# Kernel optimization log

Measured on AMD Instinct MI355X. Metric: run time of the kernel, lower is better.

Reference implementation:

```python
import jax, jax.numpy as jnp
import numpy as np

K, D, B, T = 512, 256, 32, 4096

def setup_inputs() -> dict:
    key = jax.random.key(0)
    k1, k2 = jax.random.split(key)
    z_e_x = jax.random.normal(k1, (B, D, T), dtype=jnp.float32)
    # nn.Embedding weight init uniform(-1/K, 1/K)
    emb_weight = jax.random.uniform(k2, (K, D), dtype=jnp.float32, minval=-1.0 / K, maxval=1.0 / K)
    return {"z_e_x": z_e_x, "emb_weight": emb_weight}

def reference(z_e_x, emb_weight):
    # forward(): permute [B,D,T] -> [B,T,D], nearest-codebook indices
    z = jnp.transpose(z_e_x, (0, 2, 1))  # [B, T, D]
    # squared L2 distances: ||z||^2 - 2 z.W^T + ||W||^2  -> [B, T, K]
    z_sq = jnp.sum(z * z, axis=-1, keepdims=True)           # [B, T, 1]
    w_sq = jnp.sum(emb_weight * emb_weight, axis=-1)        # [K]
    cross = jnp.einsum('btd,kd->btk', z, emb_weight)        # [B, T, K]
    dists = z_sq - 2.0 * cross + w_sq[None, None, :]
    latents = jnp.argmin(dists, axis=-1)                    # [B, T] int
    return latents
```

## Files before the change

kernel.cpp:

```cpp
#include <hip/hip_runtime.h>
#include <math.h>

#define NK 512
#define DD 256
#define NB 32
#define NT 4096

typedef __attribute__((ext_vector_type(8))) short bf16x8;
typedef __attribute__((ext_vector_type(4))) float f32x4;

#define MARGIN 1.5e-4f
#define PAD 104

__device__ __forceinline__ void bsplit(float x, unsigned short& h, unsigned short& l) {
    unsigned int u = __float_as_uint(x);
    unsigned int r = u + 0x7fffu + ((u >> 16) & 1u);
    h = (unsigned short)(r >> 16);
    float hf = __uint_as_float(((unsigned int)h) << 16);
    float res = x - hf;
    unsigned int u2 = __float_as_uint(res);
    unsigned int r2 = u2 + 0x7fffu + ((u2 >> 16) & 1u);
    l = (unsigned short)(r2 >> 16);
}

__global__ __launch_bounds__(256) void wsq_kernel(const float* __restrict__ W,
                                                  float* __restrict__ wsq) {
    int k = blockIdx.x * blockDim.x + threadIdx.x;
    if (k >= NK) return;
    const float4* row = (const float4*)(W + (size_t)k * DD);
    double s = 0.0;
    #pragma unroll 8
    for (int i = 0; i < DD / 4; ++i) {
        float4 v = row[i];
        s += (double)v.x * v.x + (double)v.y * v.y + (double)v.z * v.z + (double)v.w * v.w;
    }
    wsq[k] = (float)s;
}

__global__ __launch_bounds__(512) void convw_kernel(const float* __restrict__ W,
                                                    unsigned short* __restrict__ Wpp) {
    const int c = blockIdx.x;
    const int k = threadIdx.x;
    const int d0 = c * 32;

    float w[32];
    const float4* src4 = (const float4*)(W + (size_t)k * DD + d0);
    #pragma unroll
    for (int q = 0; q < 8; ++q) {
        float4 v = src4[q];
        w[4 * q + 0] = v.x; w[4 * q + 1] = v.y; w[4 * q + 2] = v.z; w[4 * q + 3] = v.w;
    }
    __align__(16) unsigned short o[96];
    #pragma unroll
    for (int j = 0; j < 32; ++j) {
        unsigned short h, l;
        bsplit(w[j], h, l);
        o[3 * j + 0] = h;
        o[3 * j + 1] = l;
        o[3 * j + 2] = h;
    }
    unsigned short* dst = Wpp + ((size_t)c * 512 + k) * 96;
    #pragma unroll
    for (int j = 0; j < 12; ++j) ((int4*)dst)[j] = ((const int4*)o)[j];
}

__global__ void zero_cnt(int* cnt) {
    if (threadIdx.x == 0 && blockIdx.x == 0) *cnt = 0;
}

__global__ __launch_bounds__(256, 2) void vq_phase1(const float* __restrict__ Z,
                                                    const unsigned short* __restrict__ Wpp,
                                                    const float* __restrict__ wsq,
                                                    float* __restrict__ gq1,
                                                    float* __restrict__ gq2,
                                                    int* __restrict__ gi1) {
    __shared__ __align__(16) short As[128 * PAD];
    __shared__ __align__(16) short Bs[256 * PAD];

    const int tid  = threadIdx.x;
    const int wave = tid >> 6;
    const int lane = tid & 63;
    const int lm   = lane & 15;
    const int lq   = lane >> 4;
    const int mw   = wave & 1;
    const int nw   = wave >> 1;

    const int bx = blockIdx.x;
    const int h  = bx & 1;
    const int tl = bx >> 1;
    const int b  = tl >> 5;
    const int t0 = (tl & 31) * 128;

    const int t_l = tid & 127;
    const int dg  = tid >> 7;

    const float* zcol = Z + (size_t)b * DD * NT + t0 + t_l;

    f32x4 acc[4][8];
    #pragma unroll
    for (int mt = 0; mt < 4; ++mt)
        #pragma unroll
        for (int nt = 0; nt < 8; ++nt)
            acc[mt][nt] = (f32x4){0.f, 0.f, 0.f, 0.f};

    double zacc = 0.0;

    for (int c = 0; c < 8; ++c) {
        const int d0 = c * 32;
        __syncthreads();

        {
            float zv[16];
            #pragma unroll
            for (int j = 0; j < 16; ++j)
                zv[j] = zcol[(size_t)(d0 + dg * 16 + j) * NT];
            #pragma unroll
            for (int j = 0; j < 16; ++j)
                zacc = fma((double)zv[j], (double)zv[j], zacc);

            __align__(16) unsigned int u[24];
            #pragma unroll
            for (int p = 0; p < 8; ++p) {
                int j = 2 * p;
                unsigned short h0, l0, h1, l1;
                bsplit(zv[j], h0, l0);
                bsplit(zv[j + 1], h1, l1);
                u[3 * p + 0] = (unsigned int)h0 | ((unsigned int)h0 << 16);
                u[3 * p + 1] = (unsigned int)l0 | ((unsigned int)h1 << 16);
                u[3 * p + 2] = (unsigned int)h1 | ((unsigned int)l1 << 16);
            }
            int4* dst = (int4*)&As[t_l * PAD + dg * 48];
            #pragma unroll
            for (int q = 0; q < 6; ++q) dst[q] = ((const int4*)u)[q];
        }
        {
            const unsigned short* src = Wpp + ((size_t)c * 512 + h * 256 + tid) * 96;
            int4 v[12];
            #pragma unroll
            for (int j = 0; j < 12; ++j) v[j] = ((const int4*)src)[j];
            int4* bd = (int4*)&Bs[tid * PAD];
            #pragma unroll
            for (int j = 0; j < 12; ++j) bd[j] = v[j];
        }
        __syncthreads();

        #pragma unroll
        for (int ks = 0; ks < 3; ++ks) {
            bf16x8 a[4], bb[8];
            #pragma unroll
            for (int mt = 0; mt < 4; ++mt)
                a[mt] = *(const bf16x8*)&As[(mw * 64 + mt * 16 + lm) * PAD + ks * 32 + lq * 8];
            #pragma unroll
            for (int nt = 0; nt < 8; ++nt)
                bb[nt] = *(const bf16x8*)&Bs[(nw * 128 + nt * 16 + lm) * PAD + ks * 32 + lq * 8];
            #pragma unroll
            for (int mt = 0; mt < 4; ++mt)
                #pragma unroll
                for (int nt = 0; nt < 8; ++nt)
                    acc[mt][nt] = __builtin_amdgcn_mfma_f32_16x16x32_bf16(
                        a[mt], bb[nt], acc[mt][nt], 0, 0, 0);
        }
    }

    __syncthreads();
    double* zred = (double*)As;
    zred[dg * 128 + t_l] = zacc;
    __syncthreads();
    float* zf = (float*)Bs;
    if (tid < 128) zf[tid] = (float)(zred[tid] + zred[128 + tid]);
    __syncthreads();

    float wq[8];
    #pragma unroll
    for (int nt = 0; nt < 8; ++nt)
        wq[nt] = wsq[h * 256 + nw * 128 + nt * 16 + lm];
    const int kbase = h * 256 + nw * 128 + lm;

    float* cb1 = (float*)As;
    float* cb2 = cb1 + 256;
    int*   cbi = (int*)(cb2 + 256);

    #pragma unroll
    for (int mt = 0; mt < 4; ++mt) {
        #pragma unroll
        for (int r = 0; r < 4; ++r) {
            float zz = zf[mw * 64 + mt * 16 + lq * 4 + r];
            float q1 = INFINITY, q2 = INFINITY;
            int i1 = 0x7fffffff;
            #pragma unroll
            for (int nt = 0; nt < 8; ++nt) {
                float dist = __fadd_rn(__fsub_rn(zz, __fmul_rn(2.0f, acc[mt][nt][r])), wq[nt]);
                int kk = kbase + nt * 16;
                if (dist < q1 || (dist == q1 && kk < i1)) { q2 = q1; q1 = dist; i1 = kk; }
                else if (dist < q2) q2 = dist;
            }
            #pragma unroll
            for (int mk = 1; mk <= 8; mk <<= 1) {
                float o1 = __shfl_xor(q1, mk);
                float o2 = __shfl_xor(q2, mk);
                int   oi = __shfl_xor(i1, mk);
                if (o1 < q1 || (o1 == q1 && oi < i1)) { q2 = fminf(q1, o2); q1 = o1; i1 = oi; }
                else { q2 = fminf(o1, q2); }
            }
            if (lm == 0) {
                int m = mw * 64 + mt * 16 + lq * 4 + r;
                cb1[m * 2 + nw] = q1;
                cb2[m * 2 + nw] = q2;
                cbi[m * 2 + nw] = i1;
            }
        }
    }
    __syncthreads();
    if (tid < 128) {
        float a1 = cb1[tid * 2],     a2 = cb2[tid * 2];     int ai = cbi[tid * 2];
        float b1 = cb1[tid * 2 + 1], b2 = cb2[tid * 2 + 1]; int bi = cbi[tid * 2 + 1];
        float q1, q2; int i1;
        if (b1 < a1 || (b1 == a1 && bi < ai)) { q1 = b1; i1 = bi; q2 = fminf(a1, b2); }
        else { q1 = a1; i1 = ai; q2 = fminf(b1, a2); }
        size_t bt = (size_t)b * NT + t0 + tid;
        gq1[bt * 2 + h] = q1;
        gq2[bt * 2 + h] = q2;
        gi1[bt * 2 + h] = i1;
    }
}

__global__ __launch_bounds__(256) void vq_merge(const float* __restrict__ gq1,
                                                const float* __restrict__ gq2,
                                                const int* __restrict__ gi1,
                                                int* __restrict__ out,
                                                int* __restrict__ list,
                                                int* __restrict__ cnt) {
    const int bt = blockIdx.x * 256 + threadIdx.x;
    float a1 = gq1[(size_t)bt * 2],     a2 = gq2[(size_t)bt * 2];     int ai = gi1[(size_t)bt * 2];
    float b1 = gq1[(size_t)bt * 2 + 1], b2 = gq2[(size_t)bt * 2 + 1]; int bi = gi1[(size_t)bt * 2 + 1];
    float q1, q2; int i1;
    if (b1 < a1 || (b1 == a1 && bi < ai)) { q1 = b1; i1 = bi; q2 = fminf(a1, b2); }
    else { q1 = a1; i1 = ai; q2 = fminf(b1, a2); }
    out[bt] = i1;
    if (q2 - q1 <= MARGIN) {
        int idx = atomicAdd(cnt, 1);
        list[idx] = bt;
    }
}

__global__ __launch_bounds__(256) void vq_fix(const float* __restrict__ Z,
                                              const float* __restrict__ W,
                                              const float* __restrict__ wsq,
                                              const int* __restrict__ list,
                                              const int* __restrict__ cnt,
                                              int* __restrict__ out) {
    __shared__ float  Zs[8][256];
    __shared__ double pz[8][32];
    __shared__ float  zsqs[8];
    __shared__ int    bts[8];
    __shared__ float  rv[8][4];
    __shared__ int    ri[8][4];

    const int n    = *cnt;
    const int tid  = threadIdx.x;
    const int lane = tid & 63;
    const int wv   = tid >> 6;

    for (int base = blockIdx.x * 8; base < n; base += gridDim.x * 8) {
        const int m = (n - base < 8) ? (n - base) : 8;
        __syncthreads();
        if (tid < 8) bts[tid] = list[base + ((tid < m) ? tid : 0)];
        __syncthreads();

        #pragma unroll
        for (int i = 0; i < 8; ++i) {
            if (i < m) {
                int bt = bts[i];
                int bb = bt >> 12, t = bt & 4095;
                Zs[i][tid] = Z[(size_t)bb * DD * NT + (size_t)tid * NT + t];
            }
        }
        __syncthreads();

        {
            int i = tid >> 5, seg = tid & 31;
            double s = 0.0;
            #pragma unroll
            for (int j = 0; j < 8; ++j) {
                double zz = (double)Zs[i][seg * 8 + j];
                s = fma(zz, zz, s);
            }
            pz[i][seg] = s;
        }
        __syncthreads();
        if (tid < 8) {
            double s = 0.0;
            #pragma unroll
            for (int j = 0; j < 32; ++j) s += pz[tid][j];
            zsqs[tid] = (float)s;
        }
        __syncthreads();

        float da[2][8];
        #pragma unroll
        for (int rr = 0; rr < 2; ++rr) {
            int k = tid + rr * 256;
            const float4* wr = (const float4*)(W + (size_t)k * DD);
            float a8[8];
            #pragma unroll
            for (int i = 0; i < 8; ++i) a8[i] = 0.f;
            for (int q = 0; q < 64; ++q) {
                float4 w4 = wr[q];
                #pragma unroll
                for (int i = 0; i < 8; ++i) {
                    a8[i] = fmaf(Zs[i][4 * q + 0], w4.x, a8[i]);
                    a8[i] = fmaf(Zs[i][4 * q + 1], w4.y, a8[i]);
                    a8[i] = fmaf(Zs[i][4 * q + 2], w4.z, a8[i]);
                    a8[i] = fmaf(Zs[i][4 * q + 3], w4.w, a8[i]);
                }
            }
            float wqv = wsq[k];
            #pragma unroll
            for (int i = 0; i < 8; ++i)
                da[rr][i] = __fadd_rn(__fsub_rn(zsqs[i], __fmul_rn(2.0f, a8[i])), wqv);
        }

        #pragma unroll
        for (int i = 0; i < 8; ++i) {
            float v = da[0][i]; int ix = tid;
            if (da[1][i] < v) { v = da[1][i]; ix = tid + 256; }
            #pragma unroll
            for (int mk = 1; mk <= 32; mk <<= 1) {
                float ov = __shfl_xor(v, mk);
                int   oi = __shfl_xor(ix, mk);
                if (ov < v || (ov == v && oi < ix)) { v = ov; ix = oi; }
            }
            if (lane == 0) { rv[i][wv] = v; ri[i][wv] = ix; }
        }
        __syncthreads();
        if (tid < 8 && tid < m) {
            float v = INFINITY; int ix = 0x7fffffff;
            #pragma unroll
            for (int w = 0; w < 4; ++w) {
                if (rv[tid][w] < v || (rv[tid][w] == v && ri[tid][w] < ix)) {
                    v = rv[tid][w]; ix = ri[tid][w];
                }
            }
            out[bts[tid]] = ix;
        }
    }
}

#define BT 128
#define BK 128
#define DCHUNK 32
#define NKC (NK / BK)
#define NDC (DD / DCHUNK)
#define WSTR (BK + 4)

__global__ __launch_bounds__(256) void vq_fallback(const float* __restrict__ Z,
                                                   const float* __restrict__ W,
                                                   const float* __restrict__ wsq_g,
                                                   int* __restrict__ out) {
    __shared__ __align__(16) float Zs[DCHUNK * BT];
    __shared__ __align__(16) float Ws[DCHUNK * WSTR];
    __shared__ float wsqs[NK];

    const int tid = threadIdx.x;
    const int tx  = tid & 15;
    const int ty  = tid >> 4;
    const int b   = blockIdx.y;
    const int t0  = blockIdx.x * BT;

    if (wsq_g) {
        wsqs[tid]       = wsq_g[tid];
        wsqs[tid + 256] = wsq_g[tid + 256];
    } else {
        for (int k = tid; k < NK; k += 256) {
            const float4* row = (const float4*)(W + (size_t)k * DD);
            double s = 0.0;
            for (int i = 0; i < DD / 4; ++i) {
                float4 v = row[i];
                s += (double)v.x * v.x + (double)v.y * v.y + (double)v.z * v.z + (double)v.w * v.w;
            }
            wsqs[k] = (float)s;
        }
    }

    const float* Zb = Z + (size_t)b * DD * NT + t0;

    float best[8]; int bidx[8];
    #pragma unroll
    for (int a = 0; a < 8; ++a) { best[a] = INFINITY; bidx[a] = 0x7fffffff; }
    double zsqd[8];
    #pragma unroll
    for (int a = 0; a < 8; ++a) zsqd[a] = 0.0;
    float zsqf[8];

    for (int kc = 0; kc < NKC; ++kc) {
        float acc[8][8];
        #pragma unroll
        for (int a = 0; a < 8; ++a)
            #pragma unroll
            for (int c = 0; c < 8; ++c) acc[a][c] = 0.f;

        for (int dc = 0; dc < NDC; ++dc) {
            const int d0 = dc * DCHUNK;
            __syncthreads();
            #pragma unroll
            for (int i = 0; i < 4; ++i) {
                int f  = tid + i * 256;
                int r  = f >> 5;
                int c4 = f & 31;
                float4 v = *(const float4*)(Zb + (size_t)(d0 + r) * NT + c4 * 4);
                *(float4*)(&Zs[r * BT + c4 * 4]) = v;
            }
            #pragma unroll
            for (int i = 0; i < 4; ++i) {
                int u  = tid + i * 256;
                int k  = u >> 3;
                int rg = u & 7;
                float4 v = *(const float4*)(W + (size_t)(kc * BK + k) * DD + d0 + rg * 4);
                Ws[(rg * 4 + 0) * WSTR + k] = v.x;
                Ws[(rg * 4 + 1) * WSTR + k] = v.y;
                Ws[(rg * 4 + 2) * WSTR + k] = v.z;
                Ws[(rg * 4 + 3) * WSTR + k] = v.w;
            }
            __syncthreads();
            #pragma unroll 4
            for (int d = 0; d < DCHUNK; ++d) {
                float4 z0 = *(const float4*)(&Zs[d * BT + ty * 8]);
                float4 z1 = *(const float4*)(&Zs[d * BT + ty * 8 + 4]);
                float4 w0 = *(const float4*)(&Ws[d * WSTR + tx * 8]);
                float4 w1 = *(const float4*)(&Ws[d * WSTR + tx * 8 + 4]);
                float za[8] = {z0.x, z0.y, z0.z, z0.w, z1.x, z1.y, z1.z, z1.w};
                float wa[8] = {w0.x, w0.y, w0.z, w0.w, w1.x, w1.y, w1.z, w1.w};
                if (kc == 0) {
                    #pragma unroll
                    for (int a = 0; a < 8; ++a)
                        zsqd[a] = fma((double)za[a], (double)za[a], zsqd[a]);
                }
                #pragma unroll
                for (int a = 0; a < 8; ++a)
                    #pragma unroll
                    for (int c = 0; c < 8; ++c)
                        acc[a][c] = fmaf(za[a], wa[c], acc[a][c]);
            }
        }
        if (kc == 0) {
            #pragma unroll
            for (int a = 0; a < 8; ++a) zsqf[a] = (float)zsqd[a];
        }
        #pragma unroll
        for (int c = 0; c < 8; ++c) {
            int   kg = kc * BK + tx * 8 + c;
            float wqv = wsqs[kg];
            #pragma unroll
            for (int a = 0; a < 8; ++a) {
                float c2   = __fmul_rn(2.0f, acc[a][c]);
                float s    = __fsub_rn(zsqf[a], c2);
                float dist = __fadd_rn(s, wqv);
                if (dist < best[a] || (dist == best[a] && kg < bidx[a])) {
                    best[a] = dist; bidx[a] = kg;
                }
            }
        }
    }
    __syncthreads();
    float* redv = Zs;
    int*   redi = (int*)Ws;
    #pragma unroll
    for (int a = 0; a < 8; ++a) {
        int tl2 = ty * 8 + a;
        redv[tl2 * 16 + tx] = best[a];
        redi[tl2 * 16 + tx] = bidx[a];
    }
    __syncthreads();
    if (tid < BT) {
        float bv = INFINITY; int bi = 0x7fffffff;
        #pragma unroll
        for (int j = 0; j < 16; ++j) {
            float v = redv[tid * 16 + j];
            int   i = redi[tid * 16 + j];
            if (v < bv || (v == bv && i < bi)) { bv = v; bi = i; }
        }
        out[(size_t)b * NT + t0 + tid] = bi;
    }
}

extern "C" void kernel_launch(void* const* d_in, const int* in_sizes, int n_in,
                              void* d_out, int out_size, void* d_ws, size_t ws_size,
                              hipStream_t stream) {
    const float* Z = (const float*)d_in[0];
    const float* W = (const float*)d_in[1];
    int* out = (int*)d_out;

    const size_t OFF_WSQ  = 0;
    const size_t OFF_CNT  = 2048;
    const size_t OFF_LIST = 4096;
    const size_t OFF_WPP  = OFF_LIST + 524288;
    const size_t OFF_GQ1  = OFF_WPP + 786432;
    const size_t OFF_GQ2  = OFF_GQ1 + 1048576;
    const size_t OFF_GI1  = OFF_GQ2 + 1048576;
    const size_t NEED     = OFF_GI1 + 1048576;

    if (ws_size >= NEED) {
        float* wsq = (float*)((char*)d_ws + OFF_WSQ);
        int*   cnt = (int*)((char*)d_ws + OFF_CNT);
        int*   list = (int*)((char*)d_ws + OFF_LIST);
        unsigned short* wpp = (unsigned short*)((char*)d_ws + OFF_WPP);
        float* gq1 = (float*)((char*)d_ws + OFF_GQ1);
        float* gq2 = (float*)((char*)d_ws + OFF_GQ2);
        int*   gi1 = (int*)((char*)d_ws + OFF_GI1);

        wsq_kernel<<<dim3(2), dim3(256), 0, stream>>>(W, wsq);
        convw_kernel<<<dim3(8), dim3(512), 0, stream>>>(W, wpp);
        zero_cnt<<<dim3(1), dim3(64), 0, stream>>>(cnt);
        vq_phase1<<<dim3(2048), dim3(256), 0, stream>>>(Z, wpp, wsq, gq1, gq2, gi1);
        vq_merge<<<dim3(512), dim3(256), 0, stream>>>(gq1, gq2, gi1, out, list, cnt);
        vq_fix<<<dim3(1024), dim3(256), 0, stream>>>(Z, W, wsq, list, cnt, out);
    } else {
        float* wsq = nullptr;
        if (ws_size >= NK * sizeof(float)) {
            wsq = (float*)d_ws;
            wsq_kernel<<<dim3(2), dim3(256), 0, stream>>>(W, wsq);
        }
        vq_fallback<<<dim3(NT / BT, NB), dim3(256), 0, stream>>>(Z, W, wsq, out);
    }
}
```

Before: 406.7 us.

## Switch to scaled fp16 two-term split and fuse merge with fix kernel

```diff
diff --git a/kernel.cpp b/kernel.cpp
--- a/kernel.cpp
+++ b/kernel.cpp
@@ -6,66 +6,55 @@
 #define NB 32
 #define NT 4096
 
-typedef __attribute__((ext_vector_type(8))) short bf16x8;
+typedef __attribute__((ext_vector_type(8))) _Float16 f16x8;
 typedef __attribute__((ext_vector_type(4))) float f32x4;
 
 #define MARGIN 1.5e-4f
-#define PAD 104
-
-__device__ __forceinline__ void bsplit(float x, unsigned short& h, unsigned short& l) {
-    unsigned int u = __float_as_uint(x);
-    unsigned int r = u + 0x7fffu + ((u >> 16) & 1u);
-    h = (unsigned short)(r >> 16);
-    float hf = __uint_as_float(((unsigned int)h) << 16);
-    float res = x - hf;
-    unsigned int u2 = __float_as_uint(res);
-    unsigned int r2 = u2 + 0x7fffu + ((u2 >> 16) & 1u);
-    l = (unsigned short)(r2 >> 16);
-}
-
-__global__ __launch_bounds__(256) void wsq_kernel(const float* __restrict__ W,
-                                                  float* __restrict__ wsq) {
-    int k = blockIdx.x * blockDim.x + threadIdx.x;
-    if (k >= NK) return;
-    const float4* row = (const float4*)(W + (size_t)k * DD);
-    double s = 0.0;
-    #pragma unroll 8
-    for (int i = 0; i < DD / 4; ++i) {
-        float4 v = row[i];
-        s += (double)v.x * v.x + (double)v.y * v.y + (double)v.z * v.z + (double)v.w * v.w;
-    }
-    wsq[k] = (float)s;
-}
-
-__global__ __launch_bounds__(512) void convw_kernel(const float* __restrict__ W,
-                                                    unsigned short* __restrict__ Wpp) {
-    const int c = blockIdx.x;
-    const int k = threadIdx.x;
-    const int d0 = c * 32;
-
-    float w[32];
-    const float4* src4 = (const float4*)(W + (size_t)k * DD + d0);
-    #pragma unroll
-    for (int q = 0; q < 8; ++q) {
-        float4 v = src4[q];
-        w[4 * q + 0] = v.x; w[4 * q + 1] = v.y; w[4 * q + 2] = v.z; w[4 * q + 3] = v.w;
-    }
-    __align__(16) unsigned short o[96];
-    #pragma unroll
-    for (int j = 0; j < 32; ++j) {
-        unsigned short h, l;
-        bsplit(w[j], h, l);
-        o[3 * j + 0] = h;
-        o[3 * j + 1] = l;
-        o[3 * j + 2] = h;
-    }
-    unsigned short* dst = Wpp + ((size_t)c * 512 + k) * 96;
-    #pragma unroll
-    for (int j = 0; j < 12; ++j) ((int4*)dst)[j] = ((const int4*)o)[j];
-}
-
-__global__ void zero_cnt(int* cnt) {
-    if (threadIdx.x == 0 && blockIdx.x == 0) *cnt = 0;
+#define DCH 16
+#define NCH 16
+#define KPC 32
+#define APAD 40
+
+__device__ __forceinline__ unsigned short f16bits(float x) {
+    _Float16 h = (_Float16)x;
+    unsigned short s;
+    __builtin_memcpy(&s, &h, 2);
+    return s;
+}
+
+__global__ __launch_bounds__(512) void prep_kernel(const float* __restrict__ W,
+                                                   unsigned short* __restrict__ Wpp,
+                                                   float* __restrict__ wsq) {
+    const int bx = blockIdx.x;
+    const int k  = threadIdx.x;
+    if (bx < NCH) {
+        const int d0 = bx * DCH;
+        float w[16];
+        const float4* src4 = (const float4*)(W + (size_t)k * DD + d0);
+        #pragma unroll
+        for (int q = 0; q < 4; ++q) {
+            float4 v = src4[q];
+            w[4 * q + 0] = v.x; w[4 * q + 1] = v.y; w[4 * q + 2] = v.z; w[4 * q + 3] = v.w;
+        }
+        __align__(16) unsigned int dw[16];
+        #pragma unroll
+        for (int j = 0; j < 16; ++j) {
+            unsigned short s = f16bits(w[j] * 4096.0f);
+            dw[j] = (unsigned int)s | ((unsigned int)s << 16);
+        }
+        unsigned short* dst = Wpp + ((size_t)bx * 512 + k) * 32;
+        #pragma unroll
+        for (int j = 0; j < 4; ++j) ((int4*)dst)[j] = ((const int4*)dw)[j];
+    } else {
+        const float4* row = (const float4*)(W + (size_t)k * DD);
+        double s = 0.0;
+        #pragma unroll 8
+        for (int i = 0; i < DD / 4; ++i) {
+            float4 v = row[i];
+            s += (double)v.x * v.x + (double)v.y * v.y + (double)v.z * v.z + (double)v.w * v.w;
+        }
+        wsq[k] = (float)s;
+    }
 }
 
 __global__ __launch_bounds__(256, 2) void vq_phase1(const float* __restrict__ Z,
@@ -74,8 +63,8 @@
                                                     float* __restrict__ gq1,
                                                     float* __restrict__ gq2,
                                                     int* __restrict__ gi1) {
-    __shared__ __align__(16) short As[128 * PAD];
-    __shared__ __align__(16) short Bs[256 * PAD];
+    __shared__ __align__(16) short As[128 * APAD];
+    __shared__ __align__(16) short Bs[256 * APAD];
 
     const int tid  = threadIdx.x;
     const int wave = tid >> 6;
@@ -105,61 +94,57 @@
 
     double zacc = 0.0;
 
-    for (int c = 0; c < 8; ++c) {
-        const int d0 = c * 32;
+    for (int c = 0; c < NCH; ++c) {
+        const int d0 = c * DCH;
         __syncthreads();
 
         {
-            float zv[16];
-            #pragma unroll
-            for (int j = 0; j < 16; ++j)
-                zv[j] = zcol[(size_t)(d0 + dg * 16 + j) * NT];
-            #pragma unroll
-            for (int j = 0; j < 16; ++j)
+            float zv[8];
+            #pragma unroll
+            for (int j = 0; j < 8; ++j)
+                zv[j] = zcol[(size_t)(d0 + dg * 8 + j) * NT];
+            #pragma unroll
+            for (int j = 0; j < 8; ++j)
                 zacc = fma((double)zv[j], (double)zv[j], zacc);
 
-            __align__(16) unsigned int u[24];
-            #pragma unroll
-            for (int p = 0; p < 8; ++p) {
-                int j = 2 * p;
-                unsigned short h0, l0, h1, l1;
-                bsplit(zv[j], h0, l0);
-                bsplit(zv[j + 1], h1, l1);
-                u[3 * p + 0] = (unsigned int)h0 | ((unsigned int)h0 << 16);
-                u[3 * p + 1] = (unsigned int)l0 | ((unsigned int)h1 << 16);
-                u[3 * p + 2] = (unsigned int)h1 | ((unsigned int)l1 << 16);
-            }
-            int4* dst = (int4*)&As[t_l * PAD + dg * 48];
-            #pragma unroll
-            for (int q = 0; q < 6; ++q) dst[q] = ((const int4*)u)[q];
+            __align__(16) unsigned int u[8];
+            #pragma unroll
+            for (int j = 0; j < 8; ++j) {
+                _Float16 zh = (_Float16)zv[j];
+                float rz = zv[j] - (float)zh;
+                unsigned short hs, ls;
+                __builtin_memcpy(&hs, &zh, 2);
+                ls = f16bits(rz);
+                u[j] = (unsigned int)hs | ((unsigned int)ls << 16);
+            }
+            int4* dst = (int4*)&As[t_l * APAD + dg * 16];
+            dst[0] = ((const int4*)u)[0];
+            dst[1] = ((const int4*)u)[1];
         }
         {
-            const unsigned short* src = Wpp + ((size_t)c * 512 + h * 256 + tid) * 96;
-            int4 v[12];
-            #pragma unroll
-            for (int j = 0; j < 12; ++j) v[j] = ((const int4*)src)[j];
-            int4* bd = (int4*)&Bs[tid * PAD];
-            #pragma unroll
-            for (int j = 0; j < 12; ++j) bd[j] = v[j];
-        }
-        __syncthreads();
-
-        #pragma unroll
-        for (int ks = 0; ks < 3; ++ks) {
-            bf16x8 a[4], bb[8];
-            #pragma unroll
-            for (int mt = 0; mt < 4; ++mt)
-                a[mt] = *(const bf16x8*)&As[(mw * 64 + mt * 16 + lm) * PAD + ks * 32 + lq * 8];
+            const unsigned short* src = Wpp + ((size_t)c * 512 + h * 256 + tid) * 32;
+            int4 v0 = ((const int4*)src)[0];
+            int4 v1 = ((const int4*)src)[1];
+            int4 v2 = ((const int4*)src)[2];
+            int4 v3 = ((const int4*)src)[3];
+            int4* bd = (int4*)&Bs[tid * APAD];
+            bd[0] = v0; bd[1] = v1; bd[2] = v2; bd[3] = v3;
+        }
+        __syncthreads();
+
+        f16x8 a[4], bb[8];
+        #pragma unroll
+        for (int mt = 0; mt < 4; ++mt)
+            a[mt] = *(const f16x8*)&As[(mw * 64 + mt * 16 + lm) * APAD + lq * 8];
+        #pragma unroll
+        for (int nt = 0; nt < 8; ++nt)
+            bb[nt] = *(const f16x8*)&Bs[(nw * 128 + nt * 16 + lm) * APAD + lq * 8];
+        #pragma unroll
+        for (int mt = 0; mt < 4; ++mt)
             #pragma unroll
             for (int nt = 0; nt < 8; ++nt)
-                bb[nt] = *(const bf16x8*)&Bs[(nw * 128 + nt * 16 + lm) * PAD + ks * 32 + lq * 8];
-            #pragma unroll
-            for (int mt = 0; mt < 4; ++mt)
-                #pragma unroll
-                for (int nt = 0; nt < 8; ++nt)
-                    acc[mt][nt] = __builtin_amdgcn_mfma_f32_16x16x32_bf16(
-                        a[mt], bb[nt], acc[mt][nt], 0, 0, 0);
-        }
+                acc[mt][nt] = __builtin_amdgcn_mfma_f32_16x16x32_f16(
+                    a[mt], bb[nt], acc[mt][nt], 0, 0, 0);
     }
 
     __syncthreads();
@@ -189,7 +174,8 @@
             int i1 = 0x7fffffff;
             #pragma unroll
             for (int nt = 0; nt < 8; ++nt) {
-                float dist = __fadd_rn(__fsub_rn(zz, __fmul_rn(2.0f, acc[mt][nt][r])), wq[nt]);
+                float c2   = __fmul_rn(acc[mt][nt][r], 4.8828125e-4f);
+                float dist = __fadd_rn(__fsub_rn(zz, c2), wq[nt]);
                 int kk = kbase + nt * 16;
                 if (dist < q1 || (dist == q1 && kk < i1)) { q2 = q1; q1 = dist; i1 = kk; }
                 else if (dist < q2) q2 = dist;
@@ -224,54 +210,56 @@
     }
 }
 
-__global__ __launch_bounds__(256) void vq_merge(const float* __restrict__ gq1,
-                                                const float* __restrict__ gq2,
-                                                const int* __restrict__ gi1,
-                                                int* __restrict__ out,
-                                                int* __restrict__ list,
-                                                int* __restrict__ cnt) {
-    const int bt = blockIdx.x * 256 + threadIdx.x;
-    float a1 = gq1[(size_t)bt * 2],     a2 = gq2[(size_t)bt * 2];     int ai = gi1[(size_t)bt * 2];
-    float b1 = gq1[(size_t)bt * 2 + 1], b2 = gq2[(size_t)bt * 2 + 1]; int bi = gi1[(size_t)bt * 2 + 1];
-    float q1, q2; int i1;
-    if (b1 < a1 || (b1 == a1 && bi < ai)) { q1 = b1; i1 = bi; q2 = fminf(a1, b2); }
-    else { q1 = a1; i1 = ai; q2 = fminf(b1, a2); }
-    out[bt] = i1;
-    if (q2 - q1 <= MARGIN) {
-        int idx = atomicAdd(cnt, 1);
-        list[idx] = bt;
-    }
-}
-
-__global__ __launch_bounds__(256) void vq_fix(const float* __restrict__ Z,
-                                              const float* __restrict__ W,
-                                              const float* __restrict__ wsq,
-                                              const int* __restrict__ list,
-                                              const int* __restrict__ cnt,
-                                              int* __restrict__ out) {
-    __shared__ float  Zs[8][256];
+__global__ __launch_bounds__(256) void vq_fixmerge(const float* __restrict__ Z,
+                                                   const float* __restrict__ W,
+                                                   const float* __restrict__ wsq,
+                                                   const float* __restrict__ gq1,
+                                                   const float* __restrict__ gq2,
+                                                   const int* __restrict__ gi1,
+                                                   int* __restrict__ out) {
+    __shared__ __align__(16) float Zs[8][256];
     __shared__ double pz[8][32];
     __shared__ float  zsqs[8];
     __shared__ int    bts[8];
     __shared__ float  rv[8][4];
     __shared__ int    ri[8][4];
-
-    const int n    = *cnt;
+    __shared__ int    lcnt;
+    __shared__ int    llist[256];
+
     const int tid  = threadIdx.x;
     const int lane = tid & 63;
     const int wv   = tid >> 6;
-
-    for (int base = blockIdx.x * 8; base < n; base += gridDim.x * 8) {
+    const int bt   = blockIdx.x * 256 + tid;
+
+    if (tid == 0) lcnt = 0;
+    __syncthreads();
+
+    {
+        float a1 = gq1[(size_t)bt * 2],     a2 = gq2[(size_t)bt * 2];     int ai = gi1[(size_t)bt * 2];
+        float b1 = gq1[(size_t)bt * 2 + 1], b2 = gq2[(size_t)bt * 2 + 1]; int bi = gi1[(size_t)bt * 2 + 1];
+        float q1, q2; int i1;
+        if (b1 < a1 || (b1 == a1 && bi < ai)) { q1 = b1; i1 = bi; q2 = fminf(a1, b2); }
+        else { q1 = a1; i1 = ai; q2 = fminf(b1, a2); }
+        out[bt] = i1;
+        if (q2 - q1 <= MARGIN) {
+            int p = atomicAdd(&lcnt, 1);
+            llist[p] = bt;
+        }
+    }
+    __syncthreads();
+    const int n = lcnt;
+
+    for (int base = 0; base < n; base += 8) {
         const int m = (n - base < 8) ? (n - base) : 8;
         __syncthreads();
-        if (tid < 8) bts[tid] = list[base + ((tid < m) ? tid : 0)];
+        if (tid < 8) bts[tid] = llist[base + ((tid < m) ? tid : 0)];
         __syncthreads();
 
         #pragma unroll
         for (int i = 0; i < 8; ++i) {
             if (i < m) {
-                int bt = bts[i];
-                int bb = bt >> 12, t = bt & 4095;
+                int tb = bts[i];
+                int bb = tb >> 12, t = tb & 4095;
                 Zs[i][tid] = Z[(size_t)bb * DD * NT + (size_t)tid * NT + t];
             }
         }
@@ -308,10 +296,11 @@
                 float4 w4 = wr[q];
                 #pragma unroll
                 for (int i = 0; i < 8; ++i) {
-                    a8[i] = fmaf(Zs[i][4 * q + 0], w4.x, a8[i]);
-                    a8[i] = fmaf(Zs[i][4 * q + 1], w4.y, a8[i]);
-                    a8[i] = fmaf(Zs[i][4 * q + 2], w4.z, a8[i]);
-                    a8[i] = fmaf(Zs[i][4 * q + 3], w4.w, a8[i]);
+                    float4 z4 = *(const float4*)&Zs[i][4 * q];
+                    a8[i] = fmaf(z4.x, w4.x, a8[i]);
+                    a8[i] = fmaf(z4.y, w4.y, a8[i]);
+                    a8[i] = fmaf(z4.z, w4.z, a8[i]);
+                    a8[i] = fmaf(z4.w, w4.w, a8[i]);
                 }
             }
             float wqv = wsq[k];
@@ -355,7 +344,6 @@
 
 __global__ __launch_bounds__(256) void vq_fallback(const float* __restrict__ Z,
                                                    const float* __restrict__ W,
-                                                   const float* __restrict__ wsq_g,
                                                    int* __restrict__ out) {
     __shared__ __align__(16) float Zs[DCHUNK * BT];
     __shared__ __align__(16) float Ws[DCHUNK * WSTR];
@@ -367,19 +355,14 @@
     const int b   = blockIdx.y;
     const int t0  = blockIdx.x * BT;
 
-    if (wsq_g) {
-        wsqs[tid]       = wsq_g[tid];
-        wsqs[tid + 256] = wsq_g[tid + 256];
-    } else {
-        for (int k = tid; k < NK; k += 256) {
-            const float4* row = (const float4*)(W + (size_t)k * DD);
-            double s = 0.0;
-            for (int i = 0; i < DD / 4; ++i) {
-                float4 v = row[i];
-                s += (double)v.x * v.x + (double)v.y * v.y + (double)v.z * v.z + (double)v.w * v.w;
-            }
-            wsqs[k] = (float)s;
-        }
+    for (int k = tid; k < NK; k += 256) {
+        const float4* row = (const float4*)(W + (size_t)k * DD);
+        double s = 0.0;
+        for (int i = 0; i < DD / 4; ++i) {
+            float4 v = row[i];
+            s += (double)v.x * v.x + (double)v.y * v.y + (double)v.z * v.z + (double)v.w * v.w;
+        }
+        wsqs[k] = (float)s;
     }
 
     const float* Zb = Z + (size_t)b * DD * NT + t0;
@@ -490,36 +473,24 @@
     const float* W = (const float*)d_in[1];
     int* out = (int*)d_out;
 
-    const size_t OFF_WSQ  = 0;
-    const size_t OFF_CNT  = 2048;
-    const size_t OFF_LIST = 4096;
-    const size_t OFF_WPP  = OFF_LIST + 524288;
-    const size_t OFF_GQ1  = OFF_WPP + 786432;
-    const size_t OFF_GQ2  = OFF_GQ1 + 1048576;
-    const size_t OFF_GI1  = OFF_GQ2 + 1048576;
-    const size_t NEED     = OFF_GI1 + 1048576;
+    const size_t OFF_WSQ = 0;
+    const size_t OFF_WPP = 2048;
+    const size_t OFF_GQ1 = OFF_WPP + 524288;
+    const size_t OFF_GQ2 = OFF_GQ1 + 1048576;
+    const size_t OFF_GI1 = OFF_GQ2 + 1048576;
+    const size_t NEED    = OFF_GI1 + 1048576;
 
     if (ws_size >= NEED) {
         float* wsq = (float*)((char*)d_ws + OFF_WSQ);
-        int*   cnt = (int*)((char*)d_ws + OFF_CNT);
-        int*   list = (int*)((char*)d_ws + OFF_LIST);
         unsigned short* wpp = (unsigned short*)((char*)d_ws + OFF_WPP);
         float* gq1 = (float*)((char*)d_ws + OFF_GQ1);
         float* gq2 = (float*)((char*)d_ws + OFF_GQ2);
         int*   gi1 = (int*)((char*)d_ws + OFF_GI1);
 
-        wsq_kernel<<<dim3(2), dim3(256), 0, stream>>>(W, wsq);
-        convw_kernel<<<dim3(8), dim3(512), 0, stream>>>(W, wpp);
-        zero_cnt<<<dim3(1), dim3(64), 0, stream>>>(cnt);
+        prep_kernel<<<dim3(NCH + 1), dim3(512), 0, stream>>>(W, wpp, wsq);
         vq_phase1<<<dim3(2048), dim3(256), 0, stream>>>(Z, wpp, wsq, gq1, gq2, gi1);
-        vq_merge<<<dim3(512), dim3(256), 0, stream>>>(gq1, gq2, gi1, out, list, cnt);
-        vq_fix<<<dim3(1024), dim3(256), 0, stream>>>(Z, W, wsq, list, cnt, out);
+        vq_fixmerge<<<dim3(512), dim3(256), 0, stream>>>(Z, W, wsq, gq1, gq2, gi1, out);
     } else {
-        float* wsq = nullptr;
-        if (ws_size >= NK * sizeof(float)) {
-            wsq = (float*)d_ws;
-            wsq_kernel<<<dim3(2), dim3(256), 0, stream>>>(W, wsq);
-        }
-        vq_fallback<<<dim3(NT / BT, NB), dim3(256), 0, stream>>>(Z, W, wsq, out);
-    }
-}
+        vq_fallback<<<dim3(NT / BT, NB), dim3(256), 0, stream>>>(Z, W, out);
+    }
+}
```

After: 391.4 us. 1.04x faster.
